# Kernel optimization log

Hardware: AMD Instinct MI355X
Metric: run time of the kernel (lower is better)

Reference implementation:

```python
import jax, jax.numpy as jnp
import numpy as np

N_QUBITS = 12
B = 256

# ISWAP gate, reshaped to rank-4 tensor (out1,out2,in1,in2). ISWAP is symmetric
# under qubit exchange so wire ordering does not matter.
ISWAP = jnp.asarray(
    np.array([[1, 0, 0, 0],
              [0, 0, 1j, 0],
              [0, 1j, 0, 0],
              [0, 0, 0, 1]], dtype=np.complex64).reshape(2, 2, 2, 2))


def _rx(t):
    c = jnp.cos(t * 0.5).astype(jnp.complex64)
    js = (-1j) * jnp.sin(t * 0.5).astype(jnp.complex64)
    return jnp.stack([jnp.stack([c, js]), jnp.stack([js, c])])


def _ry(t):
    c = jnp.cos(t * 0.5).astype(jnp.complex64)
    s = jnp.sin(t * 0.5).astype(jnp.complex64)
    return jnp.stack([jnp.stack([c, -s]), jnp.stack([s, c])])


def _apply1(state, U, w):
    # state: (2,)*12 with axis i = wire i
    return jnp.moveaxis(jnp.tensordot(U, state, axes=[[1], [w]]), 0, w)


def _apply2(state, U, w1, w2):
    return jnp.moveaxis(jnp.tensordot(U, state, axes=[[2, 3], [w1, w2]]), (0, 1), (w1, w2))


def _circuit(angles, weights):
    # angles: (6,6) conv features, weights: (3,) trainable rotation angles
    state = jnp.zeros((2,) * N_QUBITS, jnp.complex64).at[(0,) * N_QUBITS].set(1.0)
    for i in range(6):
        r = angles[i]
        state = _apply1(state, _rx(r[0]), 2 * i)
        state = _apply1(state, _ry(r[1]), 2 * i)
        state = _apply1(state, _rx(r[2]), 2 * i)
        state = _apply1(state, _rx(r[3]), 2 * i + 1)
        state = _apply1(state, _ry(r[4]), 2 * i + 1)
        state = _apply1(state, _rx(r[5]), 2 * i + 1)
    # iswap_layer(ascending=True): wires [11,10],[10,9],...,[1,0]
    for i in range(N_QUBITS - 1):
        state = _apply2(state, ISWAP, N_QUBITS - i - 1, N_QUBITS - i - 2)
    for i in range(6):
        r = angles[i]
        state = _apply1(state, _ry(r[0]), 2 * i)
        state = _apply1(state, _rx(r[1]), 2 * i)
        state = _apply1(state, _ry(r[2]), 2 * i)
        state = _apply1(state, _ry(r[3]), 2 * i + 1)
        state = _apply1(state, _rx(r[4]), 2 * i + 1)
        state = _apply1(state, _ry(r[5]), 2 * i + 1)
    # iswap_layer(ascending=False): wires [1,0],[2,1],...,[11,10]
    for i in range(N_QUBITS - 1):
        state = _apply2(state, ISWAP, i + 1, i)
    state = _apply1(state, _rx(weights[0]), 0)
    state = _apply1(state, _ry(weights[1]), 0)
    state = _apply1(state, _rx(weights[2]), 0)
    # expval of projectors |0><0| and |1><1| on wire 0 (zero_label / one_label)
    probs = jnp.sum(jnp.abs(state) ** 2, axis=tuple(range(1, N_QUBITS)))  # (2,)
    return probs


def setup_inputs() -> dict:
    key = jax.random.key(0)
    k1, k2, k3, k4 = jax.random.split(key, 4)
    x = jax.random.normal(k1, (B, 1, 14, 14), dtype=jnp.float32)
    conv_w = jax.random.uniform(k2, (1, 1, 4, 4), dtype=jnp.float32) * 0.1
    conv_b = jax.random.uniform(k3, (1,), dtype=jnp.float32) * 0.99 + 0.01
    q_weights = jax.random.uniform(k4, (3,), dtype=jnp.float32) * (np.pi / 2)
    return {"x": x, "conv_w": conv_w, "conv_b": conv_b, "q_weights": q_weights}


def reference(x, conv_w, conv_b, q_weights):
    bs = x.shape[0]
    y = jax.lax.conv_general_dilated(x, conv_w, window_strides=(2, 2), padding='VALID')
    y = y + conv_b[None, :, None, None]
    angles = y.reshape(bs, 6, 6)
    # Both label-0 and label-1 circuits apply the same unitary; only the
    probs = jax.vmap(_circuit, in_axes=(0, None))(angles, q_weights)  # (bs, 2)
    f1 = probs[:, 0:1]  # <|0><0|> (zero label)
    f2 = probs[:, 1:2]  # <|1><1|> (one label)
    return jnp.concatenate([f1, f2], axis=1)
```

## Files before the change

### kernel.cpp

```cpp
#include <hip/hip_runtime.h>

__device__ __forceinline__ float2 mkc(float a, float b) { float2 r; r.x = a; r.y = b; return r; }
__device__ __forceinline__ float2 cmul(float2 a, float2 b) {
    return mkc(a.x * b.x - a.y * b.y, a.x * b.y + a.y * b.x);
}
__device__ __forceinline__ float2 cadd(float2 a, float2 b) { return mkc(a.x + b.x, a.y + b.y); }

__device__ __forceinline__ float2 irot(float2 v, int m) {
    switch (m & 3) {
        case 0:  return v;
        case 1:  return mkc(-v.y, v.x);
        case 2:  return mkc(-v.x, -v.y);
        default: return mkc(v.y, -v.x);
    }
}

struct cmat { float2 m[4]; };

__device__ __forceinline__ cmat mmul(const cmat& A, const cmat& B) {
    cmat R;
    R.m[0] = cadd(cmul(A.m[0], B.m[0]), cmul(A.m[1], B.m[2]));
    R.m[1] = cadd(cmul(A.m[0], B.m[1]), cmul(A.m[1], B.m[3]));
    R.m[2] = cadd(cmul(A.m[2], B.m[0]), cmul(A.m[3], B.m[2]));
    R.m[3] = cadd(cmul(A.m[2], B.m[1]), cmul(A.m[3], B.m[3]));
    return R;
}
__device__ __forceinline__ cmat rxm(float t) {
    float c = cosf(0.5f * t), s = sinf(0.5f * t);
    cmat R; R.m[0] = mkc(c, 0.f); R.m[1] = mkc(0.f, -s); R.m[2] = mkc(0.f, -s); R.m[3] = mkc(c, 0.f);
    return R;
}
__device__ __forceinline__ cmat rym(float t) {
    float c = cosf(0.5f * t), s = sinf(0.5f * t);
    cmat R; R.m[0] = mkc(c, 0.f); R.m[1] = mkc(-s, 0.f); R.m[2] = mkc(s, 0.f); R.m[3] = mkc(c, 0.f);
    return R;
}

template<int J>
__device__ __forceinline__ void gate16(float2 (&a)[16], float2 g0, float2 g1, float2 g2, float2 g3) {
    #pragma unroll
    for (int m = 0; m < 16; ++m) {
        if (!(m & (1 << J))) {
            float2 s0 = a[m], s1 = a[m | (1 << J)];
            a[m]            = cadd(cmul(g0, s0), cmul(g1, s1));
            a[m | (1 << J)] = cadd(cmul(g2, s0), cmul(g3, s1));
        }
    }
}

__global__ __launch_bounds__(256) void qcnn_kernel(
    const float* __restrict__ x,
    const float* __restrict__ conv_w,
    const float* __restrict__ conv_b,
    const float* __restrict__ qw,
    float* __restrict__ out)
{
    __shared__ float  ang[36];
    __shared__ float2 c0s[12][2];
    __shared__ float2 g10m[4];
    __shared__ float2 g11m[4];
    __shared__ float2 Wm[4];
    __shared__ float2 KT[16];
    __shared__ float  redp[8];

    const int b = blockIdx.x;
    const int t = threadIdx.x;

    if (t < 36) {
        int oy = t / 6, ox = t % 6;
        const float* xb = x + b * 196;
        float acc = conv_b[0];
        #pragma unroll
        for (int ky = 0; ky < 4; ++ky)
            #pragma unroll
            for (int kx = 0; kx < 4; ++kx)
                acc += xb[(oy * 2 + ky) * 14 + (ox * 2 + kx)] * conv_w[ky * 4 + kx];
        ang[t] = acc;
    }
    __syncthreads();

    if (t < 12) {
        int i   = t >> 1;
        int off = (t & 1) * 3;
        float a0 = ang[i * 6 + off], a1 = ang[i * 6 + off + 1], a2 = ang[i * 6 + off + 2];
        cmat U1 = mmul(rxm(a2), mmul(rym(a1), rxm(a0)));
        c0s[t][0] = U1.m[0];
        c0s[t][1] = U1.m[2];
        if (t < 2) {
            cmat U2 = mmul(rym(a2), mmul(rxm(a1), rym(a0)));
            float2* dst = (t == 0) ? g11m : g10m;
            dst[0] = U2.m[0]; dst[1] = U2.m[1]; dst[2] = U2.m[2]; dst[3] = U2.m[3];
        }
    } else if (t == 12) {
        cmat W = mmul(rxm(qw[2]), mmul(rym(qw[1]), rxm(qw[0])));
        Wm[0] = W.m[0]; Wm[1] = W.m[1]; Wm[2] = W.m[2]; Wm[3] = W.m[3];
    }
    __syncthreads();

    if (t < 16) {
        int k = t;
        float2 v = cmul(cmul(c0s[2][k & 1], c0s[1][(k >> 1) & 1]),
                        cmul(c0s[0][(k >> 2) & 1], c0s[11][(k >> 3) & 1]));
        int pck = __popc(k & 7);
        int e = ((k < 8) ? pck : (11 - pck)) & 3;
        KT[k] = irot(v, e);
    }
    __syncthreads();

    float2 Bp = c0s[10][t & 1];
    #pragma unroll
    for (int j = 1; j < 8; ++j)
        Bp = cmul(Bp, c0s[10 - j][(t >> j) & 1]);
    int pcT = __popc(t) & 3;
    float2 P = irot(Bp, pcT);
    float2 Q = irot(Bp, (4 - pcT) & 3);

    float2 a[16];
    #pragma unroll
    for (int k = 0; k < 16; ++k)
        a[k] = cmul((k < 8) ? P : Q, KT[k]);

    gate16<2>(a, g10m[0], g10m[1], g10m[2], g10m[3]);
    gate16<3>(a, g11m[0], g11m[1], g11m[2], g11m[3]);

    #pragma unroll
    for (int m = 0; m < 4; ++m) {
        float2 u = a[m | 4], v = a[m | 8];
        a[m | 4] = mkc(-v.y, v.x);
        a[m | 8] = mkc(-u.y, u.x);
    }

    float p0 = 0.f, p1 = 0.f;
    {
        float2 w0 = Wm[0], w1 = Wm[1], w2 = Wm[2], w3 = Wm[3];
        #pragma unroll
        for (int k = 0; k < 8; ++k) {
            float2 s0 = a[k], s1 = a[k | 8];
            float2 n0 = cadd(cmul(w0, s0), cmul(w1, s1));
            float2 n1 = cadd(cmul(w2, s0), cmul(w3, s1));
            p0 += n0.x * n0.x + n0.y * n0.y;
            p1 += n1.x * n1.x + n1.y * n1.y;
        }
    }

    #pragma unroll
    for (int off = 32; off >= 1; off >>= 1) {
        p0 += __shfl_down(p0, off);
        p1 += __shfl_down(p1, off);
    }
    int wid = t >> 6;
    if ((t & 63) == 0) { redp[wid] = p0; redp[4 + wid] = p1; }
    __syncthreads();
    if (t == 0) {
        out[b * 2 + 0] = redp[0] + redp[1] + redp[2] + redp[3];
        out[b * 2 + 1] = redp[4] + redp[5] + redp[6] + redp[7];
    }
}

extern "C" void kernel_launch(void* const* d_in, const int* in_sizes, int n_in,
                              void* d_out, int out_size, void* d_ws, size_t ws_size,
                              hipStream_t stream) {
    const float* x      = (const float*)d_in[0];
    const float* conv_w = (const float*)d_in[1];
    const float* conv_b = (const float*)d_in[2];
    const float* qw     = (const float*)d_in[3];
    float* out          = (float*)d_out;

    int B = in_sizes[0] / 196;
    qcnn_kernel<<<dim3(B), dim3(256), 0, stream>>>(x, conv_w, conv_b, qw, out);
}
```

Before: 11.03 us.

## Collapse circuit to closed-form per-wire probabilities in a single wavefront

Replaces the per-thread 16-amplitude state simulation over 4096 basis states with an analytic reduction: the interior wires contribute only through products of per-wire probability terms, which are combined with xor-shuffles, leaving a 4-term phase sum handled by four lanes. The block shrinks from 256 to 64 threads and all shared memory and __syncthreads are replaced by wavefront shuffles. It also switches to the fast __sincosf intrinsic, which trades some accuracy. The work is now latency-bound on a single wave per batch element.

```diff
diff --git a/kernel.cpp b/kernel.cpp
--- a/kernel.cpp
+++ b/kernel.cpp
@@ -5,14 +5,13 @@
     return mkc(a.x * b.x - a.y * b.y, a.x * b.y + a.y * b.x);
 }
 __device__ __forceinline__ float2 cadd(float2 a, float2 b) { return mkc(a.x + b.x, a.y + b.y); }
-
+__device__ __forceinline__ float2 muli(float2 a) { return mkc(-a.y, a.x); }
 __device__ __forceinline__ float2 irot(float2 v, int m) {
-    switch (m & 3) {
-        case 0:  return v;
-        case 1:  return mkc(-v.y, v.x);
-        case 2:  return mkc(-v.x, -v.y);
-        default: return mkc(v.y, -v.x);
-    }
+    m &= 3;
+    if (m == 1) return mkc(-v.y, v.x);
+    if (m == 2) return mkc(-v.x, -v.y);
+    if (m == 3) return mkc(v.y, -v.x);
+    return v;
 }
 
 struct cmat { float2 m[4]; };
@@ -26,134 +25,137 @@
     return R;
 }
 __device__ __forceinline__ cmat rxm(float t) {
-    float c = cosf(0.5f * t), s = sinf(0.5f * t);
+    float c, s; __sincosf(0.5f * t, &s, &c);
     cmat R; R.m[0] = mkc(c, 0.f); R.m[1] = mkc(0.f, -s); R.m[2] = mkc(0.f, -s); R.m[3] = mkc(c, 0.f);
     return R;
 }
 __device__ __forceinline__ cmat rym(float t) {
-    float c = cosf(0.5f * t), s = sinf(0.5f * t);
+    float c, s; __sincosf(0.5f * t, &s, &c);
     cmat R; R.m[0] = mkc(c, 0.f); R.m[1] = mkc(-s, 0.f); R.m[2] = mkc(s, 0.f); R.m[3] = mkc(c, 0.f);
     return R;
 }
 
-template<int J>
-__device__ __forceinline__ void gate16(float2 (&a)[16], float2 g0, float2 g1, float2 g2, float2 g3) {
-    #pragma unroll
-    for (int m = 0; m < 16; ++m) {
-        if (!(m & (1 << J))) {
-            float2 s0 = a[m], s1 = a[m | (1 << J)];
-            a[m]            = cadd(cmul(g0, s0), cmul(g1, s1));
-            a[m | (1 << J)] = cadd(cmul(g2, s0), cmul(g3, s1));
-        }
-    }
+__device__ __forceinline__ void rxryrx_col0(float a0, float a1, float a2, float2& A, float2& B) {
+    float s0, c0, s1, c1, s2, c2;
+    __sincosf(0.5f * a0, &s0, &c0);
+    __sincosf(0.5f * a1, &s1, &c1);
+    __sincosf(0.5f * a2, &s2, &c2);
+    float2 A1 = mkc(c1 * c0,  s1 * s0);
+    float2 B1 = mkc(s1 * c0, -c1 * s0);
+    A = mkc(c2 * A1.x + s2 * B1.y, c2 * A1.y - s2 * B1.x);
+    B = mkc(c2 * B1.x + s2 * A1.y, c2 * B1.y - s2 * A1.x);
 }
 
-__global__ __launch_bounds__(256) void qcnn_kernel(
+__global__ __launch_bounds__(64) void qcnn_kernel(
     const float* __restrict__ x,
     const float* __restrict__ conv_w,
     const float* __restrict__ conv_b,
     const float* __restrict__ qw,
     float* __restrict__ out)
 {
-    __shared__ float  ang[36];
-    __shared__ float2 c0s[12][2];
-    __shared__ float2 g10m[4];
-    __shared__ float2 g11m[4];
-    __shared__ float2 Wm[4];
-    __shared__ float2 KT[16];
-    __shared__ float  redp[8];
-
     const int b = blockIdx.x;
     const int t = threadIdx.x;
 
+    float ang = 0.f;
     if (t < 36) {
-        int oy = t / 6, ox = t % 6;
-        const float* xb = x + b * 196;
+        int oy = t / 6, ox = t - oy * 6;
+        const float* xb = x + b * 196 + oy * 28 + ox * 2;
         float acc = conv_b[0];
         #pragma unroll
         for (int ky = 0; ky < 4; ++ky)
             #pragma unroll
             for (int kx = 0; kx < 4; ++kx)
-                acc += xb[(oy * 2 + ky) * 14 + (ox * 2 + kx)] * conv_w[ky * 4 + kx];
-        ang[t] = acc;
-    }
-    __syncthreads();
-
-    if (t < 12) {
-        int i   = t >> 1;
-        int off = (t & 1) * 3;
-        float a0 = ang[i * 6 + off], a1 = ang[i * 6 + off + 1], a2 = ang[i * 6 + off + 2];
-        cmat U1 = mmul(rxm(a2), mmul(rym(a1), rxm(a0)));
-        c0s[t][0] = U1.m[0];
-        c0s[t][1] = U1.m[2];
-        if (t < 2) {
-            cmat U2 = mmul(rym(a2), mmul(rxm(a1), rym(a0)));
-            float2* dst = (t == 0) ? g11m : g10m;
-            dst[0] = U2.m[0]; dst[1] = U2.m[1]; dst[2] = U2.m[2]; dst[3] = U2.m[3];
-        }
-    } else if (t == 12) {
-        cmat W = mmul(rxm(qw[2]), mmul(rym(qw[1]), rxm(qw[0])));
-        Wm[0] = W.m[0]; Wm[1] = W.m[1]; Wm[2] = W.m[2]; Wm[3] = W.m[3];
-    }
-    __syncthreads();
-
-    if (t < 16) {
-        int k = t;
-        float2 v = cmul(cmul(c0s[2][k & 1], c0s[1][(k >> 1) & 1]),
-                        cmul(c0s[0][(k >> 2) & 1], c0s[11][(k >> 3) & 1]));
-        int pck = __popc(k & 7);
-        int e = ((k < 8) ? pck : (11 - pck)) & 3;
-        KT[k] = irot(v, e);
-    }
-    __syncthreads();
-
-    float2 Bp = c0s[10][t & 1];
-    #pragma unroll
-    for (int j = 1; j < 8; ++j)
-        Bp = cmul(Bp, c0s[10 - j][(t >> j) & 1]);
-    int pcT = __popc(t) & 3;
-    float2 P = irot(Bp, pcT);
-    float2 Q = irot(Bp, (4 - pcT) & 3);
-
-    float2 a[16];
-    #pragma unroll
-    for (int k = 0; k < 16; ++k)
-        a[k] = cmul((k < 8) ? P : Q, KT[k]);
-
-    gate16<2>(a, g10m[0], g10m[1], g10m[2], g10m[3]);
-    gate16<3>(a, g11m[0], g11m[1], g11m[2], g11m[3]);
-
-    #pragma unroll
-    for (int m = 0; m < 4; ++m) {
-        float2 u = a[m | 4], v = a[m | 8];
-        a[m | 4] = mkc(-v.y, v.x);
-        a[m | 8] = mkc(-u.y, u.x);
+                acc += xb[ky * 14 + kx] * conv_w[ky * 4 + kx];
+        ang = acc;
     }
 
-    float p0 = 0.f, p1 = 0.f;
+    float a00 = __shfl(ang, 0),  a01 = __shfl(ang, 1),  a02 = __shfl(ang, 2);
+    float a10 = __shfl(ang, 3),  a11 = __shfl(ang, 4),  a12 = __shfl(ang, 5);
+    float aB0 = __shfl(ang, 33), aB1 = __shfl(ang, 34), aB2 = __shfl(ang, 35);
+
+    int base = (t < 12) ? ((t >> 1) * 6 + (t & 1) * 3) : 0;
+    float g0 = __shfl(ang, base), g1 = __shfl(ang, base + 1), g2 = __shfl(ang, base + 2);
+
+    float2 termC = mkc(1.f, 0.f);
+    float  termR = 1.f;
+    if (t >= 1 && t <= 10) {
+        float2 A, B; rxryrx_col0(g0, g1, g2, A, B);
+        float q0 = A.x * A.x + A.y * A.y;
+        float q1 = B.x * B.x + B.y * B.y;
+        termC = mkc(q0, q1);
+        termR = q0 - q1;
+    }
+    #pragma unroll
+    for (int m = 1; m < 16; m <<= 1) {
+        float2 o = mkc(__shfl_xor(termC.x, m, 16), __shfl_xor(termC.y, m, 16));
+        float  orr = __shfl_xor(termR, m, 16);
+        termC = cmul(termC, o);
+        termR *= orr;
+    }
+    float Gi_re = termC.x, Gi_im = termC.y, Gm = termR;
+
+    float2 v10_0, v10_1; rxryrx_col0(a00, a01, a02, v10_0, v10_1);
+    float2 v11_0, v11_1; rxryrx_col0(aB0, aB1, aB2, v11_0, v11_1);
+    cmat G11 = mmul(rym(a02), mmul(rxm(a01), rym(a00)));
+    cmat G10 = mmul(rym(a12), mmul(rxm(a11), rym(a10)));
+    cmat W   = mmul(rxm(qw[2]), mmul(rym(qw[1]), rxm(qw[0])));
+
+    int r = t & 3;
+    float sgn = (r & 1) ? -1.f : 1.f;
+    float re2 = (r == 0) ?  2.f * Gi_re :
+                (r == 1) ?  2.f * Gi_im :
+                (r == 2) ? -2.f * Gi_re : -2.f * Gi_im;
+    float Sr = 0.25f * (1.f + sgn * Gm + re2);
+
+    float2 cr  = mkc((r == 0) ? 1.f : (r == 2) ? -1.f : 0.f,
+                     (r == 1) ? 1.f : (r == 3) ? -1.f : 0.f);
+    float2 crc = mkc(cr.x, -cr.y);
+
+    float2 p00 = cmul(v10_0, v11_0);
+    float2 p10 = cmul(v10_1, v11_0);
+    float2 p01 = cmul(v10_0, v11_1);
+    float2 p11 = cmul(v10_1, v11_1);
+    float2 s0 = cmul(cr,  p00);
+    float2 s1 = cmul(cr,  muli(p10));
+    float2 s2 = cmul(crc, irot(p01, 3));
+    float2 s3 = cmul(crc, irot(p11, 2));
+
     {
-        float2 w0 = Wm[0], w1 = Wm[1], w2 = Wm[2], w3 = Wm[3];
-        #pragma unroll
-        for (int k = 0; k < 8; ++k) {
-            float2 s0 = a[k], s1 = a[k | 8];
-            float2 n0 = cadd(cmul(w0, s0), cmul(w1, s1));
-            float2 n1 = cadd(cmul(w2, s0), cmul(w3, s1));
-            p0 += n0.x * n0.x + n0.y * n0.y;
-            p1 += n1.x * n1.x + n1.y * n1.y;
-        }
+        float2 n0 = cadd(cmul(G10.m[0], s0), cmul(G10.m[1], s1));
+        float2 n1 = cadd(cmul(G10.m[2], s0), cmul(G10.m[3], s1));
+        float2 n2 = cadd(cmul(G10.m[0], s2), cmul(G10.m[1], s3));
+        float2 n3 = cadd(cmul(G10.m[2], s2), cmul(G10.m[3], s3));
+        s0 = n0; s1 = n1; s2 = n2; s3 = n3;
+    }
+    {
+        float2 n0 = cadd(cmul(G11.m[0], s0), cmul(G11.m[1], s2));
+        float2 n2 = cadd(cmul(G11.m[2], s0), cmul(G11.m[3], s2));
+        float2 n1 = cadd(cmul(G11.m[0], s1), cmul(G11.m[1], s3));
+        float2 n3 = cadd(cmul(G11.m[2], s1), cmul(G11.m[3], s3));
+        s0 = n0; s1 = n1; s2 = n2; s3 = n3;
+    }
+    {
+        float2 u = s1, v = s2;
+        s1 = muli(v);
+        s2 = muli(u);
+    }
+    float T0, T1;
+    {
+        float2 n00 = cadd(cmul(W.m[0], s0), cmul(W.m[1], s2));
+        float2 n01 = cadd(cmul(W.m[0], s1), cmul(W.m[1], s3));
+        float2 n10 = cadd(cmul(W.m[2], s0), cmul(W.m[3], s2));
+        float2 n11 = cadd(cmul(W.m[2], s1), cmul(W.m[3], s3));
+        T0 = n00.x * n00.x + n00.y * n00.y + n01.x * n01.x + n01.y * n01.y;
+        T1 = n10.x * n10.x + n10.y * n10.y + n11.x * n11.x + n11.y * n11.y;
     }
 
-    #pragma unroll
-    for (int off = 32; off >= 1; off >>= 1) {
-        p0 += __shfl_down(p0, off);
-        p1 += __shfl_down(p1, off);
-    }
-    int wid = t >> 6;
-    if ((t & 63) == 0) { redp[wid] = p0; redp[4 + wid] = p1; }
-    __syncthreads();
+    float p0 = Sr * T0, p1 = Sr * T1;
+    p0 += __shfl_xor(p0, 1, 4);  p0 += __shfl_xor(p0, 2, 4);
+    p1 += __shfl_xor(p1, 1, 4);  p1 += __shfl_xor(p1, 2, 4);
+
     if (t == 0) {
-        out[b * 2 + 0] = redp[0] + redp[1] + redp[2] + redp[3];
-        out[b * 2 + 1] = redp[4] + redp[5] + redp[6] + redp[7];
+        out[b * 2 + 0] = p0;
+        out[b * 2 + 1] = p1;
     }
 }
 
@@ -167,5 +169,5 @@
     float* out          = (float*)d_out;
 
     int B = in_sizes[0] / 196;
-    qcnn_kernel<<<dim3(B), dim3(256), 0, stream>>>(x, conv_w, conv_b, qw, out);
+    qcnn_kernel<<<dim3(B), dim3(64), 0, stream>>>(x, conv_w, conv_b, qw, out);
 }
```

Result: faster. 9.655 us (-12.5%).
